# Performance work log

Measured on AMD Instinct MI355X. Metric: run time of the kernel, lower is better.

The kernel has to match this reference:

```python
import jax, jax.numpy as jnp
import numpy as np

# Ternary quant: brevitas 2-bit narrow-range signed int quant with const scale 1.0
# -> q(x) = clamp(round(x), -1, 1), values in {-1, 0, 1}

def ternary(x):
    return jnp.clip(jnp.round(x), -1.0, 1.0)

def batchnorm(x, gamma, beta, eps=1e-5):
    # training-mode BatchNorm1d: batch statistics over dim 0 (biased var)
    mean = jnp.mean(x, axis=0)
    var = jnp.var(x, axis=0)
    return (x - mean) * jax.lax.rsqrt(var + eps) * gamma + beta

def tensornorm(x, w, b, eps=1e-4):
    # BNN-PYNQ TensorNorm: normalize over whole tensor (unbiased var), scalar affine
    mean = jnp.mean(x)
    var = jnp.var(x, ddof=1)
    return (x - mean) / jnp.sqrt(var + eps) * w + b


def setup_inputs() -> dict:
    key = jax.random.key(0)
    ks = jax.random.split(key, 4)
    B = 16384
    x = jax.random.uniform(ks[0], (B, 784), dtype=jnp.float32)          # MNIST-like in [0,1]
    W1 = 2.0 * jax.random.uniform(ks[1], (1024, 784), dtype=jnp.float32) - 1.0  # uniform(-1,1)
    W2 = 2.0 * jax.random.uniform(ks[2], (10, 1024), dtype=jnp.float32) - 1.0
    tnk1, tnk2 = jax.random.split(ks[3])
    return {
        "x": x,
        "W1": W1,
        "gamma1": jnp.ones((1024,), jnp.float32),
        "beta1": jnp.zeros((1024,), jnp.float32),
        "W2": W2,
        "gamma2": jnp.ones((10,), jnp.float32),
        "beta2": jnp.zeros((10,), jnp.float32),
        "tn_w": jax.random.uniform(tnk1, (1,), dtype=jnp.float32),
        "tn_b": jax.random.uniform(tnk2, (1,), dtype=jnp.float32),
    }


def reference(x, W1, gamma1, beta1, W2, gamma2, beta2, tn_w, tn_b):
    h = x.reshape(x.shape[0], -1)
    h = 2.0 * h - 1.0                 # input rescale to [-1,1]
    h = ternary(h)                    # QuantIdentity (2-bit act)
    h = h @ ternary(W1).T             # QuantLinear 784->1024, ternary weights, no bias
    h = batchnorm(h, gamma1, beta1)   # BatchNorm1d(1024)
    h = ternary(h)                    # QuantIdentity
    h = h @ ternary(W2).T             # QuantLinear 1024->10
    h = batchnorm(h, gamma2, beta2)   # BatchNorm1d(10)
    h = ternary(h)                    # QuantIdentity
    return tensornorm(h, tn_w, tn_b)  # TensorNorm
```

## Files before the change

### kernel.cpp

```cpp
#include <hip/hip_runtime.h>
#include <stdint.h>

typedef int i32x4 __attribute__((ext_vector_type(4)));
typedef short s16x8 __attribute__((ext_vector_type(8)));
typedef unsigned long long ull;

#define BB 16384
#define KD 784
#define KP 896
#define N1 1024
#define N2 10
#define NTOT (BB * N2)

#define OFF_AQ 0ULL
#define SZ_AQ (14680064ULL)
#define OFF_W1Q (OFF_AQ + SZ_AQ)
#define SZ_W1Q (917504ULL)
#define OFF_W2Q (OFF_W1Q + SZ_W1Q)
#define SZ_W2Q (16384ULL)
#define OFF_C1 (OFF_W2Q + SZ_W2Q)
#define SZ_C1 (33554432ULL)
#define OFF_STATS (OFF_C1 + SZ_C1)
#define SZ_STATS (16384ULL)
#define OFF_C2 (OFF_STATS + SZ_STATS)
#define SZ_C2 (1048576ULL)
#define OFF_T2 (OFF_C2 + SZ_C2)
#define SZ_T2 (163840ULL)

__device__ __forceinline__ void async16(const void* g, void* l) {
  __builtin_amdgcn_global_load_lds((__attribute__((address_space(1))) void*)(void*)(g),
                                   (__attribute__((address_space(3))) void*)(l), 16, 0, 0);
}

__device__ __forceinline__ int8_t ternq(float v) {
  float q = rintf(v);
  return q > 0.5f ? 1 : (q < -0.5f ? -1 : 0);
}

__global__ void k0_quant(const float* __restrict__ x, const float* __restrict__ W1,
                         const float* __restrict__ W2, int8_t* __restrict__ Aq,
                         int8_t* __restrict__ W1q, int8_t* __restrict__ W2q,
                         int* __restrict__ stats) {
  const int TA = BB * KP / 16;
  const int TW = N1 * KP / 16;
  const int T2 = N2 * N1 / 16;
  int tid = blockIdx.x * 256 + threadIdx.x;
  if (tid < 4096) stats[tid] = 0;
  union {
    int4 v;
    int8_t b[16];
  } o;
  o.v = make_int4(0, 0, 0, 0);
  if (tid < TA) {
    int base = tid * 16;
    int r = base / KP, k = base - r * KP;
    if (k < KD) {
      const float4* xp = (const float4*)&x[r * KD + k];
#pragma unroll
      for (int g = 0; g < 4; ++g) {
        float4 f = xp[g];
        o.b[g * 4 + 0] = ternq(2.0f * f.x - 1.0f);
        o.b[g * 4 + 1] = ternq(2.0f * f.y - 1.0f);
        o.b[g * 4 + 2] = ternq(2.0f * f.z - 1.0f);
        o.b[g * 4 + 3] = ternq(2.0f * f.w - 1.0f);
      }
    }
    *(int4*)&Aq[base] = o.v;
  } else if (tid < TA + TW) {
    int base = (tid - TA) * 16;
    int r = base / KP, k = base - r * KP;
    if (k < KD) {
      const float4* wp = (const float4*)&W1[r * KD + k];
#pragma unroll
      for (int g = 0; g < 4; ++g) {
        float4 f = wp[g];
        o.b[g * 4 + 0] = ternq(f.x);
        o.b[g * 4 + 1] = ternq(f.y);
        o.b[g * 4 + 2] = ternq(f.z);
        o.b[g * 4 + 3] = ternq(f.w);
      }
    }
    *(int4*)&W1q[base] = o.v;
  } else if (tid < TA + TW + T2) {
    int base = (tid - TA - TW) * 16;
    const float4* wp = (const float4*)&W2[base];
#pragma unroll
    for (int g = 0; g < 4; ++g) {
      float4 f = wp[g];
      o.b[g * 4 + 0] = ternq(f.x);
      o.b[g * 4 + 1] = ternq(f.y);
      o.b[g * 4 + 2] = ternq(f.z);
      o.b[g * 4 + 3] = ternq(f.w);
    }
    *(int4*)&W2q[base] = o.v;
  }
}

__global__ __launch_bounds__(256, 3) void k1_gemm1(const int8_t* __restrict__ Aq,
                                                   const int8_t* __restrict__ W1q,
                                                   short* __restrict__ C1,
                                                   int* __restrict__ colsum,
                                                   ull* __restrict__ colsq) {
  __shared__ int8_t As[128 * 128];
  __shared__ int8_t Bs[128 * 128];
  __shared__ int cS[128];
  __shared__ int cQ[128];
  const int t = threadIdx.x;
  const int lane = t & 63, wave = t >> 6;
  const int wr = wave >> 1, wc = wave & 1;
  const int rowBase = blockIdx.y * 128, colBase = blockIdx.x * 128;
  if (t < 128) {
    cS[t] = 0;
    cQ[t] = 0;
  }

  i32x4 acc[4][4] = {};
  const int m = lane & 15, kc = lane >> 4;

  int srow[4], sgo[4];
#pragma unroll
  for (int s = 0; s < 4; ++s) {
    int c = t + 256 * s;
    srow[s] = c >> 3;
    sgo[s] = ((c & 7) ^ (srow[s] & 7)) * 16;
  }

  for (int kt = 0; kt < 7; ++kt) {
    __syncthreads();
    const int kb = kt * 128;
#pragma unroll
    for (int s = 0; s < 4; ++s) {
      int c = t + 256 * s;
      async16(&Aq[(size_t)(rowBase + srow[s]) * KP + kb + sgo[s]], &As[c * 16]);
      async16(&W1q[(size_t)(colBase + srow[s]) * KP + kb + sgo[s]], &Bs[c * 16]);
    }
    __syncthreads();
#pragma unroll
    for (int h = 0; h < 2; ++h) {
      i32x4 av[4], bv[4];
#pragma unroll
      for (int i = 0; i < 4; ++i) {
        int row = 64 * wr + 16 * i + m;
        av[i] = *(const i32x4*)&As[row * 128 + (((4 * h + kc) ^ (row & 7)) * 16)];
      }
#pragma unroll
      for (int j = 0; j < 4; ++j) {
        int row = 64 * wc + 16 * j + m;
        bv[j] = *(const i32x4*)&Bs[row * 128 + (((4 * h + kc) ^ (row & 7)) * 16)];
      }
#pragma unroll
      for (int i = 0; i < 4; ++i)
#pragma unroll
        for (int j = 0; j < 4; ++j)
          acc[i][j] = __builtin_amdgcn_mfma_i32_16x16x64_i8(av[i], bv[j], acc[i][j], 0, 0, 0);
    }
  }

  const int q = lane >> 4, cl = lane & 15;
#pragma unroll
  for (int j = 0; j < 4; ++j) {
    const int colLoc = 64 * wc + 16 * j + cl;
    const int col = colBase + colLoc;
    int s = 0, sq = 0;
#pragma unroll
    for (int i = 0; i < 4; ++i) {
#pragma unroll
      for (int rg = 0; rg < 4; ++rg) {
        int v = acc[i][j][rg];
        int row = rowBase + 64 * wr + 16 * i + q * 4 + rg;
        C1[(size_t)row * N1 + col] = (short)v;
        s += v;
        sq += v * v;
      }
    }
    atomicAdd(&cS[colLoc], s);
    atomicAdd(&cQ[colLoc], sq);
  }
  __syncthreads();
  if (t < 128) {
    atomicAdd(&colsum[colBase + t], cS[t]);
    atomicAdd(&colsq[colBase + t], (ull)(unsigned)cQ[t]);
  }
}

#define W2S 1040
__global__ __launch_bounds__(256) void k45_bnq_gemm2(
    const short* __restrict__ C1, const int* __restrict__ colsum, const ull* __restrict__ colsq,
    const float* __restrict__ g1, const float* __restrict__ b1, const int8_t* __restrict__ W2q,
    int* __restrict__ C2, int* __restrict__ sum2p, ull* __restrict__ sq2p) {
  __shared__ double AcS[N1];
  __shared__ double BcS[N1];
  __shared__ int8_t W2s[16 * W2S];
  __shared__ int cS[16];
  __shared__ int cQ[16];
  const int t = threadIdx.x;
  for (int i = t; i < N1; i += 256) {
    double mean = (double)colsum[i] / 16384.0;
    double var = (double)colsq[i] / 16384.0 - mean * mean;
    double a = (double)g1[i] / sqrt(var + 1e-5);
    AcS[i] = a;
    BcS[i] = (double)b1[i] - mean * a;
  }
  for (int i = t; i < 1024; i += 256) {
    int r = i >> 6, c16 = (i & 63) * 16;
    *(int4*)&W2s[r * W2S + c16] = *(const int4*)&W2q[r * N1 + c16];
  }
  if (t < 16) {
    cS[t] = 0;
    cQ[t] = 0;
  }
  __syncthreads();

  const int lane = t & 63, wave = t >> 6;
  const int m = lane & 15, kc = lane >> 4;
  const int tile = blockIdx.x * 4 + wave;
  const int rowBase = tile * 16;
  const short* arow = &C1[(size_t)(rowBase + m) * N1];

  i32x4 acc = {0, 0, 0, 0};
#pragma unroll
  for (int kt = 0; kt < 16; ++kt) {
    const int k0 = kt * 64 + kc * 16;
    s16x8 v0 = *(const s16x8*)&arow[k0];
    s16x8 v1 = *(const s16x8*)&arow[k0 + 8];
    union {
      i32x4 v;
      int8_t b[16];
    } afr;
#pragma unroll
    for (int j = 0; j < 8; ++j) {
      double z = (double)v0[j] * AcS[k0 + j] + BcS[k0 + j];
      double qq = rint(z);
      qq = qq < -1.0 ? -1.0 : (qq > 1.0 ? 1.0 : qq);
      afr.b[j] = (int8_t)qq;
    }
#pragma unroll
    for (int j = 0; j < 8; ++j) {
      double z = (double)v1[j] * AcS[k0 + 8 + j] + BcS[k0 + 8 + j];
      double qq = rint(z);
      qq = qq < -1.0 ? -1.0 : (qq > 1.0 ? 1.0 : qq);
      afr.b[8 + j] = (int8_t)qq;
    }
    i32x4 bfr = *(const i32x4*)&W2s[m * W2S + k0];
    acc = __builtin_amdgcn_mfma_i32_16x16x64_i8(afr.v, bfr, acc, 0, 0, 0);
  }

  const int col = m;
#pragma unroll
  for (int rg = 0; rg < 4; ++rg) C2[(rowBase + kc * 4 + rg) * 16 + col] = acc[rg];
  if (col < N2) {
    int s = 0, sq = 0;
#pragma unroll
    for (int rg = 0; rg < 4; ++rg) {
      int v = acc[rg];
      s += v;
      sq += v * v;
    }
    atomicAdd(&cS[col], s);
    atomicAdd(&cQ[col], sq);
  }
  __syncthreads();
  if (t < N2) {
    atomicAdd(&sum2p[t * 16], cS[t]);
    atomicAdd(&sq2p[t * 8], (ull)(unsigned)cQ[t]);
  }
}

__global__ __launch_bounds__(256) void k7_bn2q(const int* __restrict__ C2,
                                               const int* __restrict__ sum2p,
                                               const ull* __restrict__ sq2p,
                                               const float* __restrict__ g2,
                                               const float* __restrict__ b2,
                                               int8_t* __restrict__ t2, int* __restrict__ gsum,
                                               int* __restrict__ gsq) {
  int s = 0, sq = 0;
  for (int id = blockIdx.x * 256 + threadIdx.x; id < NTOT; id += gridDim.x * 256) {
    int r = id / N2, c = id - r * N2;
    int v = C2[r * 16 + c];
    double mean = (double)sum2p[c * 16] / 16384.0;
    double var = (double)sq2p[c * 8] / 16384.0 - mean * mean;
    double z = ((double)v - mean) / sqrt(var + 1e-5) * (double)g2[c] + (double)b2[c];
    double qq = rint(z);
    qq = qq < -1.0 ? -1.0 : (qq > 1.0 ? 1.0 : qq);
    int ti = (int)qq;
    t2[id] = (int8_t)ti;
    s += ti;
    sq += ti * ti;
  }
#pragma unroll
  for (int off = 32; off > 0; off >>= 1) {
    s += __shfl_xor(s, off, 64);
    sq += __shfl_xor(sq, off, 64);
  }
  __shared__ int bs, bq;
  if (threadIdx.x == 0) {
    bs = 0;
    bq = 0;
  }
  __syncthreads();
  if ((threadIdx.x & 63) == 0) {
    atomicAdd(&bs, s);
    atomicAdd(&bq, sq);
  }
  __syncthreads();
  if (threadIdx.x == 0) {
    atomicAdd(gsum, bs);
    atomicAdd(gsq, bq);
  }
}

__global__ void k9_out(const int8_t* __restrict__ t2, const int* __restrict__ gsum,
                       const int* __restrict__ gsq, const float* __restrict__ tn_w,
                       const float* __restrict__ tn_b, float* __restrict__ out) {
  int id = blockIdx.x * 256 + threadIdx.x;
  double n = (double)NTOT;
  double sm = (double)*gsum;
  double mean = sm / n;
  double var = ((double)*gsq - sm * sm / n) / (n - 1.0);
  double alpha = (double)tn_w[0] / sqrt(var + 1e-4);
  out[id] = (float)(((double)t2[id] - mean) * alpha + (double)tn_b[0]);
}

extern "C" void kernel_launch(void* const* d_in, const int* in_sizes, int n_in, void* d_out,
                              int out_size, void* d_ws, size_t ws_size, hipStream_t stream) {
  const float* x = (const float*)d_in[0];
  const float* W1 = (const float*)d_in[1];
  const float* g1 = (const float*)d_in[2];
  const float* b1 = (const float*)d_in[3];
  const float* W2 = (const float*)d_in[4];
  const float* g2 = (const float*)d_in[5];
  const float* b2 = (const float*)d_in[6];
  const float* tnw = (const float*)d_in[7];
  const float* tnb = (const float*)d_in[8];

  char* ws = (char*)d_ws;
  int8_t* Aq = (int8_t*)(ws + OFF_AQ);
  int8_t* W1q = (int8_t*)(ws + OFF_W1Q);
  int8_t* W2q = (int8_t*)(ws + OFF_W2Q);
  short* C1 = (short*)(ws + OFF_C1);
  int* statsZ = (int*)(ws + OFF_STATS);
  int* colsum = (int*)(ws + OFF_STATS);
  ull* colsq = (ull*)(ws + OFF_STATS + 4096);
  int* sum2p = (int*)(ws + OFF_STATS + 12288);
  ull* sq2p = (ull*)(ws + OFF_STATS + 13312);
  int* gsum = (int*)(ws + OFF_STATS + 14336);
  int* gsq = (int*)(ws + OFF_STATS + 14400);
  int* C2 = (int*)(ws + OFF_C2);
  int8_t* t2 = (int8_t*)(ws + OFF_T2);

  const int totalT = BB * KP / 16 + N1 * KP / 16 + N2 * N1 / 16;
  k0_quant<<<(totalT + 255) / 256, 256, 0, stream>>>(x, W1, W2, Aq, W1q, W2q, statsZ);
  k1_gemm1<<<dim3(8, 128), 256, 0, stream>>>(Aq, W1q, C1, colsum, colsq);
  k45_bnq_gemm2<<<256, 256, 0, stream>>>(C1, colsum, colsq, g1, b1, W2q, C2, sum2p, sq2p);
  k7_bn2q<<<160, 256, 0, stream>>>(C2, sum2p, sq2p, g2, b2, t2, gsum, gsq);
  k9_out<<<NTOT / 256, 256, 0, stream>>>(t2, gsum, gsq, tnw, tnb, (float*)d_out);
}
```

Measured before the change: 153.8 us.

## Replace fp64 BN+ternary with integer thresholds, shrink C2 to int16, hoist BN2 stats

The per-element fp64 batchnorm-then-ternarize in the second GEMM's A-operand path becomes a precomputed pair of integer thresholds per column plus a sign. Each element is then classified with two integer compares instead of fp64 FMA, rint and clamps. C2 is stored as int16 instead of int32 to halve its traffic, BN2 mean and std are computed once per block in shared memory, and GEMM1 launch bounds are raised to 4 waves per SIMD. Risks are threshold edge cases and int16 overflow of C2, whose values are bounded by 1024, so it is safe.

```diff
diff --git a/kernel.cpp b/kernel.cpp
--- a/kernel.cpp
+++ b/kernel.cpp
@@ -23,7 +23,7 @@
 #define OFF_STATS (OFF_C1 + SZ_C1)
 #define SZ_STATS (16384ULL)
 #define OFF_C2 (OFF_STATS + SZ_STATS)
-#define SZ_C2 (1048576ULL)
+#define SZ_C2 (524288ULL)
 #define OFF_T2 (OFF_C2 + SZ_C2)
 #define SZ_T2 (163840ULL)
 
@@ -96,7 +96,7 @@
   }
 }
 
-__global__ __launch_bounds__(256, 3) void k1_gemm1(const int8_t* __restrict__ Aq,
+__global__ __launch_bounds__(256, 4) void k1_gemm1(const int8_t* __restrict__ Aq,
                                                    const int8_t* __restrict__ W1q,
                                                    short* __restrict__ C1,
                                                    int* __restrict__ colsum,
@@ -183,13 +183,51 @@
   }
 }
 
+__device__ __forceinline__ void mk_thr(double a, double b, int& hi, int& lo, int8_t& sgn) {
+  sgn = 1;
+  if (a < 0.0) {
+    a = -a;
+    sgn = -1;
+  }
+  if (a == 0.0) {
+    double q = rint(b);
+    if (q > 0.5) {
+      hi = -1500;
+      lo = -2000;
+    } else if (q < -0.5) {
+      hi = 2000;
+      lo = 1500;
+    } else {
+      hi = 1500;
+      lo = -1500;
+    }
+    return;
+  }
+  double g = (0.5 - b) / a;
+  g = g > 1e6 ? 1e6 : (g < -1e6 ? -1e6 : g);
+  if (g != g) g = 0.0;
+  int c0 = (int)floor(g);
+  c0 = c0 < -1400 ? -1400 : (c0 > 1400 ? 1400 : c0);
+  for (int it = 0; it < 6 && fma((double)(c0 - 1), a, b) > 0.5; ++it) --c0;
+  for (int it = 0; it < 6 && fma((double)c0, a, b) <= 0.5; ++it) ++c0;
+  hi = c0 < -1500 ? -1500 : (c0 > 1500 ? 1500 : c0);
+  double g2 = (-0.5 - b) / a;
+  g2 = g2 > 1e6 ? 1e6 : (g2 < -1e6 ? -1e6 : g2);
+  if (g2 != g2) g2 = 0.0;
+  int c1 = (int)ceil(g2);
+  c1 = c1 < -1400 ? -1400 : (c1 > 1400 ? 1400 : c1);
+  for (int it = 0; it < 6 && fma((double)(c1 + 1), a, b) < -0.5; ++it) ++c1;
+  for (int it = 0; it < 6 && fma((double)c1, a, b) >= -0.5; ++it) --c1;
+  lo = c1 < -1500 ? -1500 : (c1 > 1500 ? 1500 : c1);
+}
+
 #define W2S 1040
 __global__ __launch_bounds__(256) void k45_bnq_gemm2(
     const short* __restrict__ C1, const int* __restrict__ colsum, const ull* __restrict__ colsq,
     const float* __restrict__ g1, const float* __restrict__ b1, const int8_t* __restrict__ W2q,
-    int* __restrict__ C2, int* __restrict__ sum2p, ull* __restrict__ sq2p) {
-  __shared__ double AcS[N1];
-  __shared__ double BcS[N1];
+    short* __restrict__ C2, int* __restrict__ sum2p, ull* __restrict__ sq2p) {
+  __shared__ int tpkS[N1];
+  __shared__ int8_t sgnS[N1];
   __shared__ int8_t W2s[16 * W2S];
   __shared__ int cS[16];
   __shared__ int cQ[16];
@@ -198,8 +236,12 @@
     double mean = (double)colsum[i] / 16384.0;
     double var = (double)colsq[i] / 16384.0 - mean * mean;
     double a = (double)g1[i] / sqrt(var + 1e-5);
-    AcS[i] = a;
-    BcS[i] = (double)b1[i] - mean * a;
+    double b = (double)b1[i] - mean * a;
+    int hi, lo;
+    int8_t sg;
+    mk_thr(a, b, hi, lo, sg);
+    tpkS[i] = (hi << 16) | (lo & 0xffff);
+    sgnS[i] = sg;
   }
   for (int i = t; i < 1024; i += 256) {
     int r = i >> 6, c16 = (i & 63) * 16;
@@ -224,22 +266,35 @@
     s16x8 v0 = *(const s16x8*)&arow[k0];
     s16x8 v1 = *(const s16x8*)&arow[k0 + 8];
     union {
+      int4 v[4];
+      int w[16];
+    } tps;
+    tps.v[0] = *(const int4*)&tpkS[k0];
+    tps.v[1] = *(const int4*)&tpkS[k0 + 4];
+    tps.v[2] = *(const int4*)&tpkS[k0 + 8];
+    tps.v[3] = *(const int4*)&tpkS[k0 + 12];
+    union {
+      int4 v;
+      int8_t b[16];
+    } sg;
+    sg.v = *(const int4*)&sgnS[k0];
+    union {
       i32x4 v;
       int8_t b[16];
     } afr;
 #pragma unroll
     for (int j = 0; j < 8; ++j) {
-      double z = (double)v0[j] * AcS[k0 + j] + BcS[k0 + j];
-      double qq = rint(z);
-      qq = qq < -1.0 ? -1.0 : (qq > 1.0 ? 1.0 : qq);
-      afr.b[j] = (int8_t)qq;
+      int tp = tps.w[j];
+      int hi = tp >> 16, lo = (short)(tp & 0xffff);
+      int w = (int)v0[j] * (int)sg.b[j];
+      afr.b[j] = (int8_t)((w >= hi) - (w <= lo));
     }
 #pragma unroll
     for (int j = 0; j < 8; ++j) {
-      double z = (double)v1[j] * AcS[k0 + 8 + j] + BcS[k0 + 8 + j];
-      double qq = rint(z);
-      qq = qq < -1.0 ? -1.0 : (qq > 1.0 ? 1.0 : qq);
-      afr.b[8 + j] = (int8_t)qq;
+      int tp = tps.w[8 + j];
+      int hi = tp >> 16, lo = (short)(tp & 0xffff);
+      int w = (int)v1[j] * (int)sg.b[8 + j];
+      afr.b[8 + j] = (int8_t)((w >= hi) - (w <= lo));
     }
     i32x4 bfr = *(const i32x4*)&W2s[m * W2S + k0];
     acc = __builtin_amdgcn_mfma_i32_16x16x64_i8(afr.v, bfr, acc, 0, 0, 0);
@@ -247,7 +302,7 @@
 
   const int col = m;
 #pragma unroll
-  for (int rg = 0; rg < 4; ++rg) C2[(rowBase + kc * 4 + rg) * 16 + col] = acc[rg];
+  for (int rg = 0; rg < 4; ++rg) C2[(rowBase + kc * 4 + rg) * 16 + col] = (short)acc[rg];
   if (col < N2) {
     int s = 0, sq = 0;
 #pragma unroll
@@ -266,20 +321,27 @@
   }
 }
 
-__global__ __launch_bounds__(256) void k7_bn2q(const int* __restrict__ C2,
+__global__ __launch_bounds__(256) void k7_bn2q(const short* __restrict__ C2,
                                                const int* __restrict__ sum2p,
                                                const ull* __restrict__ sq2p,
                                                const float* __restrict__ g2,
                                                const float* __restrict__ b2,
                                                int8_t* __restrict__ t2, int* __restrict__ gsum,
                                                int* __restrict__ gsq) {
+  __shared__ double meanS[N2], rsS[N2];
+  if (threadIdx.x < N2) {
+    int c = threadIdx.x;
+    double mean = (double)sum2p[c * 16] / 16384.0;
+    double var = (double)sq2p[c * 8] / 16384.0 - mean * mean;
+    meanS[c] = mean;
+    rsS[c] = sqrt(var + 1e-5);
+  }
+  __syncthreads();
   int s = 0, sq = 0;
   for (int id = blockIdx.x * 256 + threadIdx.x; id < NTOT; id += gridDim.x * 256) {
     int r = id / N2, c = id - r * N2;
     int v = C2[r * 16 + c];
-    double mean = (double)sum2p[c * 16] / 16384.0;
-    double var = (double)sq2p[c * 8] / 16384.0 - mean * mean;
-    double z = ((double)v - mean) / sqrt(var + 1e-5) * (double)g2[c] + (double)b2[c];
+    double z = ((double)v - meanS[c]) / rsS[c] * (double)g2[c] + (double)b2[c];
     double qq = rint(z);
     qq = qq < -1.0 ? -1.0 : (qq > 1.0 ? 1.0 : qq);
     int ti = (int)qq;
@@ -345,7 +407,7 @@
   ull* sq2p = (ull*)(ws + OFF_STATS + 13312);
   int* gsum = (int*)(ws + OFF_STATS + 14336);
   int* gsq = (int*)(ws + OFF_STATS + 14400);
-  int* C2 = (int*)(ws + OFF_C2);
+  short* C2 = (short*)(ws + OFF_C2);
   int8_t* t2 = (int8_t*)(ws + OFF_T2);
 
   const int totalT = BB * KP / 16 + N1 * KP / 16 + N2 * N1 / 16;
```

Measured after the change: 151.8 us. About the same (-1.3%).
